# Optimization experiments

Hardware: AMD Instinct MI355X
Metric: run time of the kernel (lower is better)

Reference implementation:

```python
import jax, jax.numpy as jnp
import numpy as np

N_NODES = 100000
N_EDGES = 6400000
HID = 32


def setup_inputs() -> dict:
    key = jax.random.key(0)
    ks = jax.random.split(key, 24)
    inp = {
        "x_G": jax.random.normal(ks[0], (N_NODES, 1), dtype=jnp.float32),
        "edge_index_G": jax.random.randint(ks[1], (2, N_EDGES), 0, N_NODES, dtype=jnp.int32),
        "x_H": jax.random.normal(ks[2], (N_NODES, 1), dtype=jnp.float32),
        "edge_index_H": jax.random.randint(ks[3], (2, N_EDGES), 0, N_NODES, dtype=jnp.int32),
    }
    ki = 4
    for i in range(3):
        d_in = 1 if i == 0 else HID
        inp[f"W1_{i}"] = jax.random.normal(ks[ki], (d_in, HID), dtype=jnp.float32) / np.sqrt(d_in); ki += 1
        inp[f"b1_{i}"] = jnp.zeros((HID,), dtype=jnp.float32)
        inp[f"W2_{i}"] = jax.random.normal(ks[ki], (HID, HID), dtype=jnp.float32) / np.sqrt(HID); ki += 1
        inp[f"b2_{i}"] = jnp.zeros((HID,), dtype=jnp.float32)
    inp["Wc1"] = jax.random.normal(ks[ki], (2 * HID, HID), dtype=jnp.float32) / np.sqrt(2 * HID); ki += 1
    inp["bc1"] = jnp.zeros((HID,), dtype=jnp.float32)
    inp["Wc2"] = jax.random.normal(ks[ki], (HID, 1), dtype=jnp.float32) / np.sqrt(HID); ki += 1
    inp["bc2"] = jnp.zeros((1,), dtype=jnp.float32)
    return inp


def _encode(x, edge_index, layers):
    n = x.shape[0]
    src, dst = edge_index[0], edge_index[1]
    for (W1, b1, W2, b2) in layers:
        # GIN aggregation: sum of neighbor messages scattered to targets; eps = 0
        agg = jax.ops.segment_sum(x[src], dst, num_segments=n)  # [N, d]
        h = x + agg  # (1 + eps) * x + agg with eps = 0
        h = jax.nn.relu(h @ W1 + b1) @ W2 + b2  # GIN MLP
        x = jax.nn.relu(h)  # outer F.relu in encode loop
    return jnp.sum(x, axis=0, keepdims=True)  # global_add_pool, single graph -> [1, HID]


def reference(x_G, edge_index_G, x_H, edge_index_H,
              W1_0, b1_0, W2_0, b2_0,
              W1_1, b1_1, W2_1, b2_1,
              W1_2, b1_2, W2_2, b2_2,
              Wc1, bc1, Wc2, bc2):
    layers = [(W1_0, b1_0, W2_0, b2_0),
              (W1_1, b1_1, W2_1, b2_1),
              (W1_2, b1_2, W2_2, b2_2)]
    h_G = _encode(x_G, edge_index_G, layers)
    h_H = _encode(x_H, edge_index_H, layers)
    combined = jnp.concatenate([h_G, h_H], axis=1)  # [1, 2*HID]
    out = jax.nn.relu(combined @ Wc1 + bc1) @ Wc2 + bc2
    return jax.nn.sigmoid(out)
```

## Files before the change

kernel.cpp:

```cpp
#include <hip/hip_runtime.h>
#include <hip/hip_bf16.h>
#include <math.h>
#include <string.h>

#define HID 32
#define PSHIFT 8
#define NPB (1 << PSHIFT)
#define MAXP 512
#define SLOTS 17408
#define SBITS 3
#define SBINS (1 << SBITS)
#define NBINS (NPB * SBINS)
#define GS 32
#define HS_ROWS 32
#define COLBUF 1536
#define COLBUF0 6144
typedef unsigned short u16;

__device__ inline float bf2f(u16 u) {
    unsigned v = ((unsigned)u) << 16;
    float f; memcpy(&f, &v, 4); return f;
}
__device__ inline u16 f2bf(float f) {
    unsigned x; memcpy(&x, &f, 4);
    unsigned r = x + 0x7fffu + ((x >> 16) & 1u);
    return (u16)(r >> 16);
}
__device__ inline void acc_bf2(float* a, unsigned w) {
    a[0] += bf2f((u16)(w & 0xffff));
    a[1] += bf2f((u16)(w >> 16));
}

__global__ void zero_kernel(float* __restrict__ p, int n) {
    int i = blockIdx.x * blockDim.x + threadIdx.x;
    if (i < n) p[i] = 0.f;
}
__global__ void init_gcur(int* __restrict__ gcur, int P) {
    int b = blockIdx.x * blockDim.x + threadIdx.x;
    if (b < P) gcur[b * GS] = b * SLOTS;
}

__global__ void partition_edges(const int* __restrict__ src, const int* __restrict__ dst,
                                int* __restrict__ gcur, unsigned* __restrict__ staged,
                                int E, int P) {
    __shared__ int h[4][MAXP];
    __shared__ int hbase[MAXP];
    __shared__ int cur[MAXP];
    __shared__ int gbase[MAXP];
    __shared__ unsigned sortedv[4096];
    __shared__ u16 bktid[4096];
    __shared__ int wsums[4];
    __shared__ int sTotal;
    int t = threadIdx.x, wid = t >> 6, lane = t & 63;
    for (int i = t; i < 4 * MAXP; i += 256) (&h[0][0])[i] = 0;
    __syncthreads();

    int base = blockIdx.x * 4096;
    int4 S[4], D[4];
#pragma unroll
    for (int r = 0; r < 4; r++) {
        int e = base + r * 1024 + t * 4;
        if (e + 3 < E) {
            S[r] = *(const int4*)(src + e);
            D[r] = *(const int4*)(dst + e);
        } else {
            int s0[4], d0[4];
            for (int j = 0; j < 4; j++) {
                int ee = e + j;
                s0[j] = (ee < E) ? src[ee] : -1;
                d0[j] = (ee < E) ? dst[ee] : -1;
            }
            S[r] = make_int4(s0[0], s0[1], s0[2], s0[3]);
            D[r] = make_int4(d0[0], d0[1], d0[2], d0[3]);
        }
        if (D[r].x >= 0) atomicAdd(&h[wid][D[r].x >> PSHIFT], 1);
        if (D[r].y >= 0) atomicAdd(&h[wid][D[r].y >> PSHIFT], 1);
        if (D[r].z >= 0) atomicAdd(&h[wid][D[r].z >> PSHIFT], 1);
        if (D[r].w >= 0) atomicAdd(&h[wid][D[r].w >> PSHIFT], 1);
    }
    __syncthreads();

    int b0 = 2 * t, b1 = 2 * t + 1;
    int t0 = (b0 < P) ? (h[0][b0] + h[1][b0] + h[2][b0] + h[3][b0]) : 0;
    int t1 = (b1 < P) ? (h[0][b1] + h[1][b1] + h[2][b1] + h[3][b1]) : 0;
    int s = t0 + t1;
    int incl = s;
#pragma unroll
    for (int off = 1; off < 64; off <<= 1) {
        int u = __shfl_up(incl, off, 64);
        if (lane >= off) incl += u;
    }
    if (lane == 63) wsums[wid] = incl;
    __syncthreads();
    int woff = 0;
#pragma unroll
    for (int w = 0; w < 4; w++) if (w < wid) woff += wsums[w];
    int excl = woff + incl - s;
    if (b0 < P) { hbase[b0] = excl;      cur[b0] = excl; }
    if (b1 < P) { hbase[b1] = excl + t0; cur[b1] = excl + t0; }
    if (b0 < P && t0) gbase[b0] = atomicAdd(&gcur[b0 * GS], t0);
    if (b1 < P && t1) gbase[b1] = atomicAdd(&gcur[b1 * GS], t1);
    if (t == 255) sTotal = excl + s;
    __syncthreads();

#pragma unroll
    for (int r = 0; r < 4; r++) {
        int ss[4] = { S[r].x, S[r].y, S[r].z, S[r].w };
        int dd[4] = { D[r].x, D[r].y, D[r].z, D[r].w };
#pragma unroll
        for (int j = 0; j < 4; j++) {
            int d = dd[j];
            if (d >= 0) {
                int bk = d >> PSHIFT;
                int pos = atomicAdd(&cur[bk], 1);
                sortedv[pos] = ((unsigned)(d & (NPB - 1)) << 17) | (unsigned)ss[j];
                bktid[pos]   = (u16)bk;
            }
        }
    }
    __syncthreads();

    int total = sTotal;
    for (int i = t; i < total; i += 256) {
        int bk = bktid[i];
        int addr = gbase[bk] + (i - hbase[bk]);
        if (addr < (bk + 1) * SLOTS)
            staged[addr] = sortedv[i];
    }
}

__global__ void scan_buckets(const int* __restrict__ gcur, int* __restrict__ colbase,
                             int* __restrict__ rowptr, int P, int N) {
    __shared__ int wsums[4];
    int t = threadIdx.x, wid = t >> 6, lane = t & 63;
    int b0 = 2 * t, b1 = 2 * t + 1;
    int c0 = 0, c1 = 0;
    if (b0 < P) { c0 = gcur[b0 * GS] - b0 * SLOTS; if (c0 > SLOTS) c0 = SLOTS; }
    if (b1 < P) { c1 = gcur[b1 * GS] - b1 * SLOTS; if (c1 > SLOTS) c1 = SLOTS; }
    int s = c0 + c1;
    int incl = s;
#pragma unroll
    for (int off = 1; off < 64; off <<= 1) {
        int u = __shfl_up(incl, off, 64);
        if (lane >= off) incl += u;
    }
    if (lane == 63) wsums[wid] = incl;
    __syncthreads();
    int woff = 0;
#pragma unroll
    for (int w = 0; w < 4; w++) if (w < wid) woff += wsums[w];
    int excl = woff + incl - s;
    if (b0 < P) colbase[b0] = excl;
    if (b1 < P) colbase[b1] = excl + c0;
    if (t == 255) {
        colbase[P] = excl + s;
        rowptr[N]  = excl + s;
    }
}

__global__ void sort_bucket(const unsigned* __restrict__ staged, const int* __restrict__ gcur,
                            const int* __restrict__ colbase,
                            int* __restrict__ rowptr, int* __restrict__ col, int N) {
    __shared__ int cnt[NBINS];
    __shared__ int wsum[4];
    __shared__ int sorted[SLOTS];
    int b = blockIdx.x;
    int t = threadIdx.x;
    int lane = t & 63, wid = t >> 6;
    int sBeg = b * SLOTS;
    int sEnd = gcur[b * GS]; if (sEnd > sBeg + SLOTS) sEnd = sBeg + SLOTS;
    int total = sEnd - sBeg;
    int colStart = colbase[b];
    int nodeBase = b << PSHIFT;

    for (int i = t; i < NBINS; i += 256) cnt[i] = 0;
    __syncthreads();
    for (int i = sBeg + t; i < sEnd; i += 256) {
        unsigned w = staged[i];
        int key = (int)((w >> 17) << SBITS) | (int)((w & 0x1FFFFu) >> 14);
        atomicAdd(&cnt[key], 1);
    }
    __syncthreads();

    int loc[SBINS]; int tot = 0;
#pragma unroll
    for (int k = 0; k < SBINS; k++) { loc[k] = tot; tot += cnt[(t << SBITS) + k]; }
    int incl = tot;
#pragma unroll
    for (int off = 1; off < 64; off <<= 1) {
        int u = __shfl_up(incl, off, 64);
        if (lane >= off) incl += u;
    }
    if (lane == 63) wsum[wid] = incl;
    __syncthreads();
    int woff = 0;
#pragma unroll
    for (int w = 0; w < 4; w++) if (w < wid) woff += wsum[w];
    int excl = woff + incl - tot;
    int node = nodeBase + t;
    if (node < N) rowptr[node] = colStart + excl;
#pragma unroll
    for (int k = 0; k < SBINS; k++) cnt[(t << SBITS) + k] = excl + loc[k];
    __syncthreads();

    for (int i = sBeg + t; i < sEnd; i += 256) {
        unsigned w = staged[i];
        int key = (int)((w >> 17) << SBITS) | (int)((w & 0x1FFFFu) >> 14);
        int pos = atomicAdd(&cnt[key], 1);
        sorted[pos] = (int)(w & 0x1FFFFu);
    }
    __syncthreads();
    for (int i = t; i < total; i += 256)
        col[colStart + i] = sorted[i];
}

__global__ void mlp0_fused(const int* __restrict__ rowptr, const int* __restrict__ col,
                           const float* __restrict__ x0,
                           const float* __restrict__ W1, const float* __restrict__ b1,
                           const float* __restrict__ W2, const float* __restrict__ b2,
                           u16* __restrict__ out, int n) {
    __shared__ float sW1[HID], sb1[HID], sW2[HID * HID], sb2[HID];
    __shared__ int colbuf[COLBUF0];
    int t = threadIdx.x;
    if (t < HID) { sW1[t] = W1[t]; sb1[t] = b1[t]; sb2[t] = b2[t]; }
    for (int i = t; i < HID * HID; i += blockDim.x) sW2[i] = W2[i];

    int firstNode = blockIdx.x * 64;
    int lastNode  = firstNode + 64; if (lastNode > n) lastNode = n;
    int blockStart = (firstNode < n) ? rowptr[firstNode] : 0;
    int blockEnd   = (firstNode < n) ? rowptr[lastNode] : 0;
    int stagedCnt = blockEnd - blockStart; if (stagedCnt > COLBUF0) stagedCnt = COLBUF0;
    for (int i = t; i < stagedCnt; i += 256) colbuf[i] = col[blockStart + i];
    __syncthreads();

    int node = firstNode + (t >> 2);
    int q    = t & 3;
    int lane = t & 63;
    int base = lane & ~3;
    bool active = node < n;

    float s = 0.f;
    if (active) {
        int beg = rowptr[node], end = rowptr[node + 1];
        int jSplit = blockStart + stagedCnt; if (jSplit > end) jSplit = end;
        int j = beg + q;
        for (; j + 12 < jSplit; j += 16) {
            int c0 = colbuf[j - blockStart];
            int c1 = colbuf[j + 4 - blockStart];
            int c2 = colbuf[j + 8 - blockStart];
            int c3 = colbuf[j + 12 - blockStart];
            s += x0[c0]; s += x0[c1]; s += x0[c2]; s += x0[c3];
        }
        for (; j < jSplit; j += 4) s += x0[colbuf[j - blockStart]];
        for (; j < end; j += 4) s += x0[col[j]];
    }
    s += __shfl_xor(s, 1, 64);
    s += __shfl_xor(s, 2, 64);
    float v = active ? (x0[node] + s) : 0.f;

    float h[8];
#pragma unroll
    for (int i = 0; i < 8; i++) h[i] = fmaxf(fmaf(v, sW1[q * 8 + i], sb1[q * 8 + i]), 0.f);
    float o[8];
#pragma unroll
    for (int i = 0; i < 8; i++) o[i] = sb2[q * 8 + i];
#pragma unroll
    for (int k = 0; k < HID; k++) {
        float hk = __shfl(h[k & 7], base | (k >> 3), 64);
#pragma unroll
        for (int i = 0; i < 8; i++) o[i] = fmaf(hk, sW2[k * HID + q * 8 + i], o[i]);
    }
    if (active) {
        union { u16 u[8]; uint4 v4; } pk;
#pragma unroll
        for (int i = 0; i < 8; i++) pk.u[i] = f2bf(fmaxf(o[i], 0.f));
        *(uint4*)(out + ((size_t)node << 5) + (q << 3)) = pk.v4;
    }
}

template <bool REDUCE>
__global__ void mlp_fused(const int* __restrict__ rowptr, const int* __restrict__ col,
                          const u16* __restrict__ xin,
                          const float* __restrict__ W1, const float* __restrict__ b1,
                          const float* __restrict__ W2, const float* __restrict__ b2,
                          u16* __restrict__ xout, float* __restrict__ hsum, int n) {
    __shared__ float sW1[HID * HID], sb1[HID], sW2[HID * HID], sb2[HID];
    __shared__ int colbuf[COLBUF];
    __shared__ float red[4][HID];
    int t = threadIdx.x;
    for (int i = t; i < HID * HID; i += blockDim.x) { sW1[i] = W1[i]; sW2[i] = W2[i]; }
    if (t < HID) { sb1[t] = b1[t]; sb2[t] = b2[t]; }

    int firstNode = blockIdx.x * 16;
    int lastNode  = firstNode + 16; if (lastNode > n) lastNode = n;
    int blockStart = (firstNode < n) ? rowptr[firstNode] : 0;
    int blockEnd   = (firstNode < n) ? rowptr[lastNode] : 0;
    int stagedCnt = blockEnd - blockStart; if (stagedCnt > COLBUF) stagedCnt = COLBUF;
    for (int i = t; i < stagedCnt; i += 256) colbuf[i] = col[blockStart + i];
    __syncthreads();

    int node = firstNode + (t >> 4);
    int q    = t & 15;
    int lane = t & 63;
    int base = lane & ~15;
    bool active = node < n;

    float va[2];
    va[0] = 0.f; va[1] = 0.f;
    if (active) {
        int beg = rowptr[node], end = rowptr[node + 1];
        const u16* xq = xin + (q << 1);
        float a0[2], a1[2], a2[2], a3[2];
#pragma unroll
        for (int i = 0; i < 2; i++) a0[i] = a1[i] = a2[i] = a3[i] = 0.f;
        {
            unsigned w = *(const unsigned*)(xq + ((size_t)node << 5));
            acc_bf2(a0, w);
        }
        int jSplit = blockStart + stagedCnt; if (jSplit > end) jSplit = end;
        int j = beg;
        for (; j + 8 <= jSplit; j += 8) {
            int lj = j - blockStart;
            int c0 = colbuf[lj+0], c1 = colbuf[lj+1], c2 = colbuf[lj+2], c3 = colbuf[lj+3];
            int c4 = colbuf[lj+4], c5 = colbuf[lj+5], c6 = colbuf[lj+6], c7 = colbuf[lj+7];
            unsigned w0 = *(const unsigned*)(xq + ((size_t)c0 << 5));
            unsigned w1 = *(const unsigned*)(xq + ((size_t)c1 << 5));
            unsigned w2 = *(const unsigned*)(xq + ((size_t)c2 << 5));
            unsigned w3 = *(const unsigned*)(xq + ((size_t)c3 << 5));
            unsigned w4 = *(const unsigned*)(xq + ((size_t)c4 << 5));
            unsigned w5 = *(const unsigned*)(xq + ((size_t)c5 << 5));
            unsigned w6 = *(const unsigned*)(xq + ((size_t)c6 << 5));
            unsigned w7 = *(const unsigned*)(xq + ((size_t)c7 << 5));
            acc_bf2(a0, w0); acc_bf2(a1, w1); acc_bf2(a2, w2); acc_bf2(a3, w3);
            acc_bf2(a0, w4); acc_bf2(a1, w5); acc_bf2(a2, w6); acc_bf2(a3, w7);
        }
        for (; j < jSplit; j++) {
            unsigned w = *(const unsigned*)(xq + ((size_t)colbuf[j - blockStart] << 5));
            acc_bf2(a0, w);
        }
        for (; j < end; j++) {
            unsigned w = *(const unsigned*)(xq + ((size_t)col[j] << 5));
            acc_bf2(a0, w);
        }
#pragma unroll
        for (int i = 0; i < 2; i++) va[i] = (a0[i] + a1[i]) + (a2[i] + a3[i]);
    }

    float h[2];
#pragma unroll
    for (int i = 0; i < 2; i++) h[i] = sb1[q * 2 + i];
#pragma unroll
    for (int k = 0; k < HID; k++) {
        float vk = __shfl(va[k & 1], base | (k >> 1), 64);
#pragma unroll
        for (int i = 0; i < 2; i++) h[i] = fmaf(vk, sW1[k * HID + q * 2 + i], h[i]);
    }
#pragma unroll
    for (int i = 0; i < 2; i++) h[i] = fmaxf(h[i], 0.f);

    float o[2];
#pragma unroll
    for (int i = 0; i < 2; i++) o[i] = sb2[q * 2 + i];
#pragma unroll
    for (int k = 0; k < HID; k++) {
        float hk = __shfl(h[k & 1], base | (k >> 1), 64);
#pragma unroll
        for (int i = 0; i < 2; i++) o[i] = fmaf(hk, sW2[k * HID + q * 2 + i], o[i]);
    }
#pragma unroll
    for (int i = 0; i < 2; i++) o[i] = fmaxf(o[i], 0.f);

    if (REDUCE) {
        if (!active) {
#pragma unroll
            for (int i = 0; i < 2; i++) o[i] = 0.f;
        }
#pragma unroll
        for (int i = 0; i < 2; i++) {
            float v = o[i];
            v += __shfl_xor(v, 16, 64);
            v += __shfl_xor(v, 32, 64);
            o[i] = v;
        }
        int wid = t >> 6;
        if (lane < 16) {
#pragma unroll
            for (int i = 0; i < 2; i++) red[wid][lane * 2 + i] = o[i];
        }
        __syncthreads();
        if (t < HID) {
            float s = red[0][t] + red[1][t] + red[2][t] + red[3][t];
            atomicAdd(&hsum[(blockIdx.x & (HS_ROWS - 1)) * (2 * HID) + t], s);
        }
    } else if (active) {
        union { u16 u[2]; unsigned w; } pk;
        pk.u[0] = f2bf(o[0]); pk.u[1] = f2bf(o[1]);
        *(unsigned*)(xout + ((size_t)node << 5) + (q << 1)) = pk.w;
    }
}

__global__ void head_kernel(const float* __restrict__ hsumP,
                            const float* __restrict__ Wc1, const float* __restrict__ bc1,
                            const float* __restrict__ Wc2, const float* __restrict__ bc2,
                            float* __restrict__ out) {
    __shared__ float hs[2 * HID];
    int t = threadIdx.x;
    if (t < 2 * HID) {
        float s = 0.f;
        for (int r = 0; r < HS_ROWS; r++) s += hsumP[r * (2 * HID) + t];
        hs[t] = s;
    }
    __syncthreads();
    float val = 0.f;
    if (t < HID) {
        float acc = bc1[t];
        for (int i = 0; i < 2 * HID; i++) acc = fmaf(hs[i], Wc1[i * HID + t], acc);
        val = fmaxf(acc, 0.f) * Wc2[t];
    }
    for (int off = 32; off >= 1; off >>= 1) val += __shfl_xor(val, off, 64);
    if (t == 0) out[0] = 1.f / (1.f + expf(-(val + bc2[0])));
}

extern "C" void kernel_launch(void* const* d_in, const int* in_sizes, int n_in,
                              void* d_out, int out_size, void* d_ws, size_t ws_size,
                              hipStream_t stream) {
    const float* xg[2] = { (const float*)d_in[0], (const float*)d_in[2] };
    const int*   eg[2] = { (const int*)d_in[1],   (const int*)d_in[3] };
    const float* W1[3] = { (const float*)d_in[4], (const float*)d_in[8],  (const float*)d_in[12] };
    const float* b1[3] = { (const float*)d_in[5], (const float*)d_in[9],  (const float*)d_in[13] };
    const float* W2[3] = { (const float*)d_in[6], (const float*)d_in[10], (const float*)d_in[14] };
    const float* b2[3] = { (const float*)d_in[7], (const float*)d_in[11], (const float*)d_in[15] };
    const float* Wc1 = (const float*)d_in[16];
    const float* bc1 = (const float*)d_in[17];
    const float* Wc2 = (const float*)d_in[18];
    const float* bc2 = (const float*)d_in[19];

    const int N = in_sizes[0];
    const int E = in_sizes[1] / 2;
    const int P = (N + NPB - 1) >> PSHIFT;

    u16*      B0      = (u16*)d_ws;
    u16*      B1      = B0 + (size_t)N * HID;
    float*    hsumP   = (float*)(B1 + (size_t)N * HID);
    int*      rowptr  = (int*)(hsumP + HS_ROWS * 2 * HID);
    int*      col     = rowptr + (N + 1);
    int*      colbase = col + (size_t)E;
    int*      gcur    = colbase + (P + 1);
    unsigned* staged  = (unsigned*)(gcur + (size_t)P * GS);

    const int TB = 256;
    dim3 blk(TB);
    int gE4k = (E + 4095) / 4096;
    int gN64 = (N + 63) / 64;
    int gN16 = (N + 15) / 16;
    int gP   = (P + TB - 1) / TB;

    zero_kernel<<<(HS_ROWS * 2 * HID + 255) / 256, 256, 0, stream>>>(hsumP, HS_ROWS * 2 * HID);

    for (int g = 0; g < 2; g++) {
        const float* x0  = xg[g];
        const int*   src = eg[g];
        const int*   dst = src + E;

        init_gcur<<<gP, blk, 0, stream>>>(gcur, P);
        partition_edges<<<gE4k, blk, 0, stream>>>(src, dst, gcur, staged, E, P);
        scan_buckets<<<1, blk, 0, stream>>>(gcur, colbase, rowptr, P, N);
        sort_bucket<<<P, blk, 0, stream>>>(staged, gcur, colbase, rowptr, col, N);

        mlp0_fused<<<gN64, blk, 0, stream>>>(rowptr, col, x0, W1[0], b1[0], W2[0], b2[0], B0, N);

        mlp_fused<false><<<gN16, blk, 0, stream>>>(rowptr, col, B0, W1[1], b1[1], W2[1], b2[1],
                                                   B1, nullptr, N);

        mlp_fused<true><<<gN16, blk, 0, stream>>>(rowptr, col, B1, W1[2], b1[2], W2[2], b2[2],
                                                  nullptr, hsumP + g * HID, N);
    }

    head_kernel<<<1, 64, 0, stream>>>(hsumP, Wc1, bc1, Wc2, bc2, (float*)d_out);
}
```

Before: 654.6 us.

## Store intermediate node features as FP8 E4M3 and halve gather traffic

After: 578.6 us. 11.6% less time.

```diff
diff --git a/kernel.cpp b/kernel.cpp
--- a/kernel.cpp
+++ b/kernel.cpp
@@ -13,22 +13,33 @@
 #define NBINS (NPB * SBINS)
 #define GS 32
 #define HS_ROWS 32
-#define COLBUF 1536
+#define COLBUF 3072
 #define COLBUF0 6144
 typedef unsigned short u16;
-
-__device__ inline float bf2f(u16 u) {
-    unsigned v = ((unsigned)u) << 16;
-    float f; memcpy(&f, &v, 4); return f;
+typedef unsigned char u8;
+
+__device__ inline float e42f(unsigned b) {
+    unsigned u = (b & 0x7fu) << 20;
+    float f; memcpy(&f, &u, 4);
+    return f * 0x1p120f;
+}
+__device__ inline unsigned f2e4(float f) {
+    f = fminf(f, 448.f);
+    float y = f * 0x1p-120f;
+    unsigned r; memcpy(&r, &y, 4);
+    r = r + 0x7FFFFu + ((r >> 20) & 1u);
+    return (r >> 20) & 0x7fu;
+}
+__device__ inline void acc_e4(float* a, unsigned w) {
+    a[0] += e42f(w);
+    a[1] += e42f(w >> 8);
+    a[2] += e42f(w >> 16);
+    a[3] += e42f(w >> 24);
 }
 __device__ inline u16 f2bf(float f) {
     unsigned x; memcpy(&x, &f, 4);
     unsigned r = x + 0x7fffu + ((x >> 16) & 1u);
     return (u16)(r >> 16);
-}
-__device__ inline void acc_bf2(float* a, unsigned w) {
-    a[0] += bf2f((u16)(w & 0xffff));
-    a[1] += bf2f((u16)(w >> 16));
 }
 
 __global__ void zero_kernel(float* __restrict__ p, int n) {
@@ -218,7 +229,7 @@
                            const float* __restrict__ x0,
                            const float* __restrict__ W1, const float* __restrict__ b1,
                            const float* __restrict__ W2, const float* __restrict__ b2,
-                           u16* __restrict__ out, int n) {
+                           u8* __restrict__ out, int n) {
     __shared__ float sW1[HID], sb1[HID], sW2[HID * HID], sb2[HID];
     __shared__ int colbuf[COLBUF0];
     int t = threadIdx.x;
@@ -271,19 +282,21 @@
         for (int i = 0; i < 8; i++) o[i] = fmaf(hk, sW2[k * HID + q * 8 + i], o[i]);
     }
     if (active) {
-        union { u16 u[8]; uint4 v4; } pk;
-#pragma unroll
-        for (int i = 0; i < 8; i++) pk.u[i] = f2bf(fmaxf(o[i], 0.f));
-        *(uint4*)(out + ((size_t)node << 5) + (q << 3)) = pk.v4;
+        unsigned w0 = f2e4(fmaxf(o[0], 0.f)) | (f2e4(fmaxf(o[1], 0.f)) << 8)
+                    | (f2e4(fmaxf(o[2], 0.f)) << 16) | (f2e4(fmaxf(o[3], 0.f)) << 24);
+        unsigned w1 = f2e4(fmaxf(o[4], 0.f)) | (f2e4(fmaxf(o[5], 0.f)) << 8)
+                    | (f2e4(fmaxf(o[6], 0.f)) << 16) | (f2e4(fmaxf(o[7], 0.f)) << 24);
+        uint2 pk = make_uint2(w0, w1);
+        *(uint2*)(out + ((size_t)node << 5) + (q << 3)) = pk;
     }
 }
 
 template <bool REDUCE>
 __global__ void mlp_fused(const int* __restrict__ rowptr, const int* __restrict__ col,
-                          const u16* __restrict__ xin,
+                          const u8* __restrict__ xin,
                           const float* __restrict__ W1, const float* __restrict__ b1,
                           const float* __restrict__ W2, const float* __restrict__ b2,
-                          u16* __restrict__ xout, float* __restrict__ hsum, int n) {
+                          u8* __restrict__ xout, float* __restrict__ hsum, int n) {
     __shared__ float sW1[HID * HID], sb1[HID], sW2[HID * HID], sb2[HID];
     __shared__ int colbuf[COLBUF];
     __shared__ float red[4][HID];
@@ -291,31 +304,32 @@
     for (int i = t; i < HID * HID; i += blockDim.x) { sW1[i] = W1[i]; sW2[i] = W2[i]; }
     if (t < HID) { sb1[t] = b1[t]; sb2[t] = b2[t]; }
 
-    int firstNode = blockIdx.x * 16;
-    int lastNode  = firstNode + 16; if (lastNode > n) lastNode = n;
+    int firstNode = blockIdx.x * 32;
+    int lastNode  = firstNode + 32; if (lastNode > n) lastNode = n;
     int blockStart = (firstNode < n) ? rowptr[firstNode] : 0;
     int blockEnd   = (firstNode < n) ? rowptr[lastNode] : 0;
     int stagedCnt = blockEnd - blockStart; if (stagedCnt > COLBUF) stagedCnt = COLBUF;
     for (int i = t; i < stagedCnt; i += 256) colbuf[i] = col[blockStart + i];
     __syncthreads();
 
-    int node = firstNode + (t >> 4);
-    int q    = t & 15;
+    int node = firstNode + (t >> 3);
+    int q    = t & 7;
     int lane = t & 63;
-    int base = lane & ~15;
+    int base = lane & ~7;
     bool active = node < n;
 
-    float va[2];
-    va[0] = 0.f; va[1] = 0.f;
+    float va[4];
+#pragma unroll
+    for (int i = 0; i < 4; i++) va[i] = 0.f;
     if (active) {
         int beg = rowptr[node], end = rowptr[node + 1];
-        const u16* xq = xin + (q << 1);
-        float a0[2], a1[2], a2[2], a3[2];
-#pragma unroll
-        for (int i = 0; i < 2; i++) a0[i] = a1[i] = a2[i] = a3[i] = 0.f;
+        const u8* xq = xin + (q << 2);
+        float a0[4], a1[4], a2[4], a3[4];
+#pragma unroll
+        for (int i = 0; i < 4; i++) a0[i] = a1[i] = a2[i] = a3[i] = 0.f;
         {
             unsigned w = *(const unsigned*)(xq + ((size_t)node << 5));
-            acc_bf2(a0, w);
+            acc_e4(a0, w);
         }
         int jSplit = blockStart + stagedCnt; if (jSplit > end) jSplit = end;
         int j = beg;
@@ -331,61 +345,62 @@
             unsigned w5 = *(const unsigned*)(xq + ((size_t)c5 << 5));
             unsigned w6 = *(const unsigned*)(xq + ((size_t)c6 << 5));
             unsigned w7 = *(const unsigned*)(xq + ((size_t)c7 << 5));
-            acc_bf2(a0, w0); acc_bf2(a1, w1); acc_bf2(a2, w2); acc_bf2(a3, w3);
-            acc_bf2(a0, w4); acc_bf2(a1, w5); acc_bf2(a2, w6); acc_bf2(a3, w7);
+            acc_e4(a0, w0); acc_e4(a1, w1); acc_e4(a2, w2); acc_e4(a3, w3);
+            acc_e4(a0, w4); acc_e4(a1, w5); acc_e4(a2, w6); acc_e4(a3, w7);
         }
         for (; j < jSplit; j++) {
             unsigned w = *(const unsigned*)(xq + ((size_t)colbuf[j - blockStart] << 5));
-            acc_bf2(a0, w);
+            acc_e4(a0, w);
         }
         for (; j < end; j++) {
             unsigned w = *(const unsigned*)(xq + ((size_t)col[j] << 5));
-            acc_bf2(a0, w);
-        }
-#pragma unroll
-        for (int i = 0; i < 2; i++) va[i] = (a0[i] + a1[i]) + (a2[i] + a3[i]);
-    }
-
-    float h[2];
-#pragma unroll
-    for (int i = 0; i < 2; i++) h[i] = sb1[q * 2 + i];
+            acc_e4(a0, w);
+        }
+#pragma unroll
+        for (int i = 0; i < 4; i++) va[i] = (a0[i] + a1[i]) + (a2[i] + a3[i]);
+    }
+
+    float h[4];
+#pragma unroll
+    for (int i = 0; i < 4; i++) h[i] = sb1[q * 4 + i];
 #pragma unroll
     for (int k = 0; k < HID; k++) {
-        float vk = __shfl(va[k & 1], base | (k >> 1), 64);
-#pragma unroll
-        for (int i = 0; i < 2; i++) h[i] = fmaf(vk, sW1[k * HID + q * 2 + i], h[i]);
-    }
-#pragma unroll
-    for (int i = 0; i < 2; i++) h[i] = fmaxf(h[i], 0.f);
-
-    float o[2];
-#pragma unroll
-    for (int i = 0; i < 2; i++) o[i] = sb2[q * 2 + i];
+        float vk = __shfl(va[k & 3], base | (k >> 2), 64);
+#pragma unroll
+        for (int i = 0; i < 4; i++) h[i] = fmaf(vk, sW1[k * HID + q * 4 + i], h[i]);
+    }
+#pragma unroll
+    for (int i = 0; i < 4; i++) h[i] = fmaxf(h[i], 0.f);
+
+    float o[4];
+#pragma unroll
+    for (int i = 0; i < 4; i++) o[i] = sb2[q * 4 + i];
 #pragma unroll
     for (int k = 0; k < HID; k++) {
-        float hk = __shfl(h[k & 1], base | (k >> 1), 64);
-#pragma unroll
-        for (int i = 0; i < 2; i++) o[i] = fmaf(hk, sW2[k * HID + q * 2 + i], o[i]);
-    }
-#pragma unroll
-    for (int i = 0; i < 2; i++) o[i] = fmaxf(o[i], 0.f);
+        float hk = __shfl(h[k & 3], base | (k >> 2), 64);
+#pragma unroll
+        for (int i = 0; i < 4; i++) o[i] = fmaf(hk, sW2[k * HID + q * 4 + i], o[i]);
+    }
+#pragma unroll
+    for (int i = 0; i < 4; i++) o[i] = fmaxf(o[i], 0.f);
 
     if (REDUCE) {
         if (!active) {
 #pragma unroll
-            for (int i = 0; i < 2; i++) o[i] = 0.f;
-        }
-#pragma unroll
-        for (int i = 0; i < 2; i++) {
+            for (int i = 0; i < 4; i++) o[i] = 0.f;
+        }
+#pragma unroll
+        for (int i = 0; i < 4; i++) {
             float v = o[i];
+            v += __shfl_xor(v, 8, 64);
             v += __shfl_xor(v, 16, 64);
             v += __shfl_xor(v, 32, 64);
             o[i] = v;
         }
         int wid = t >> 6;
-        if (lane < 16) {
-#pragma unroll
-            for (int i = 0; i < 2; i++) red[wid][lane * 2 + i] = o[i];
+        if (lane < 8) {
+#pragma unroll
+            for (int i = 0; i < 4; i++) red[wid][lane * 4 + i] = o[i];
         }
         __syncthreads();
         if (t < HID) {
@@ -393,9 +408,8 @@
             atomicAdd(&hsum[(blockIdx.x & (HS_ROWS - 1)) * (2 * HID) + t], s);
         }
     } else if (active) {
-        union { u16 u[2]; unsigned w; } pk;
-        pk.u[0] = f2bf(o[0]); pk.u[1] = f2bf(o[1]);
-        *(unsigned*)(xout + ((size_t)node << 5) + (q << 1)) = pk.w;
+        unsigned pw = f2e4(o[0]) | (f2e4(o[1]) << 8) | (f2e4(o[2]) << 16) | (f2e4(o[3]) << 24);
+        *(unsigned*)(xout + ((size_t)node << 5) + (q << 2)) = pw;
     }
 }
 
@@ -439,9 +453,9 @@
     const int E = in_sizes[1] / 2;
     const int P = (N + NPB - 1) >> PSHIFT;
 
-    u16*      B0      = (u16*)d_ws;
-    u16*      B1      = B0 + (size_t)N * HID;
-    float*    hsumP   = (float*)(B1 + (size_t)N * HID);
+    u8*       B0      = (u8*)d_ws;
+    u8*       B1      = B0 + (size_t)N * 32;
+    float*    hsumP   = (float*)(B1 + (size_t)N * 32);
     int*      rowptr  = (int*)(hsumP + HS_ROWS * 2 * HID);
     int*      col     = rowptr + (N + 1);
     int*      colbase = col + (size_t)E;
@@ -452,7 +466,7 @@
     dim3 blk(TB);
     int gE4k = (E + 4095) / 4096;
     int gN64 = (N + 63) / 64;
-    int gN16 = (N + 15) / 16;
+    int gN8  = (N + 31) / 32;
     int gP   = (P + TB - 1) / TB;
 
     zero_kernel<<<(HS_ROWS * 2 * HID + 255) / 256, 256, 0, stream>>>(hsumP, HS_ROWS * 2 * HID);
@@ -469,11 +483,11 @@
 
         mlp0_fused<<<gN64, blk, 0, stream>>>(rowptr, col, x0, W1[0], b1[0], W2[0], b2[0], B0, N);
 
-        mlp_fused<false><<<gN16, blk, 0, stream>>>(rowptr, col, B0, W1[1], b1[1], W2[1], b2[1],
-                                                   B1, nullptr, N);
-
-        mlp_fused<true><<<gN16, blk, 0, stream>>>(rowptr, col, B1, W1[2], b1[2], W2[2], b2[2],
-                                                  nullptr, hsumP + g * HID, N);
+        mlp_fused<false><<<gN8, blk, 0, stream>>>(rowptr, col, B0, W1[1], b1[1], W2[1], b2[1],
+                                                  B1, nullptr, N);
+
+        mlp_fused<true><<<gN8, blk, 0, stream>>>(rowptr, col, B1, W1[2], b1[2], W2[2], b2[2],
+                                                 nullptr, hsumP + g * HID, N);
     }
 
     head_kernel<<<1, 64, 0, stream>>>(hsumP, Wc1, bc1, Wc2, bc2, (float*)d_out);
```
